# Kernel tuning notes

Measured on AMD Instinct MI355X. Metric: run time of the kernel, lower is better.

Reference implementation:

```python
import jax, jax.numpy as jnp
import numpy as np

N = 8192
MARGIN = 0.2
LAMB = 0.012
ITERS = 5


def setup_inputs() -> dict:
    key = jax.random.key(0)
    # sims in [0,1): cosine-similarity-like scores; exp(-(1-s)/lamb) needs s near [0,1]
    sims = jax.random.uniform(key, (N, N), dtype=jnp.float32)
    return {"sims": sims}


def _ot(sims):
    # Sinkhorn-Knopp normalization, r = c = ones so (r/u) == 1/u, (c/v) == 1/v
    P = jnp.exp(-(1.0 - sims) / LAMB)
    P = P / jnp.sum(P)  # global normalization (dims [-2,-1])
    for _ in range(ITERS):
        u = P.sum(axis=-1, keepdims=True)   # row sums  [N,1]
        P = P / u
        v = P.sum(axis=-2, keepdims=True)   # col sums  [1,N]
        P = P / v
    return P


def reference(sims):
    P = _ot(sims)
    d = jnp.diagonal(P)                     # [N]
    eye = jnp.eye(P.shape[0], dtype=bool)
    # cost_im: anchor = column diagonal (d[j]); cost_s: anchor = row diagonal (d[i])
    cost_im = jnp.where(eye, 0.0, jnp.maximum(P - d[None, :] + MARGIN, 0.0))
    cost_s = jnp.where(eye, 0.0, jnp.maximum(P - d[:, None] + MARGIN, 0.0))
    # max_violation = False -> sum over all hinge terms
    return cost_s.sum() + cost_im.sum()
```

## Files before the change

kernel.cpp:

```cpp
#include <hip/hip_runtime.h>


#define NN 8192u
#define MARGIN 0.2f
#define KF (1.4426950408889634f / 0.012f)

typedef float f32x4 __attribute__((ext_vector_type(4)));

__device__ __forceinline__ float wave_sum(float v) {
#pragma unroll
  for (int off = 32; off; off >>= 1) v += __shfl_down(v, off, 64);
  return v;
}


__global__ __launch_bounds__(256) void k_pass0(const float* __restrict__ sims,
                                               uint* __restrict__ Qd,
                                               float* __restrict__ R,
                                               float* __restrict__ qdiag,
                                               float* __restrict__ out) {
  __shared__ float red[4];
  const uint row = blockIdx.x, t = threadIdx.x;
  const uint lane = t & 63u, wid = t >> 6;
  if (row == 0u && t == 0u) *out = 0.f;
  float acc = 0.f;
#pragma unroll
  for (uint ch = 0; ch < 8u; ++ch) {
    const uint col0 = ch * 1024u + t * 4u;
    const f32x4 s = __builtin_nontemporal_load(
        (const f32x4*)(sims + (size_t)row * NN + col0));
    int p = 0;
    p = __builtin_amdgcn_cvt_pk_fp8_f32(exp2f((s[0] - 1.f) * KF),
                                        exp2f((s[1] - 1.f) * KF), p, false);
    p = __builtin_amdgcn_cvt_pk_fp8_f32(exp2f((s[2] - 1.f) * KF),
                                        exp2f((s[3] - 1.f) * KF), p, true);
    const uint up = (uint)p;
    Qd[((size_t)row * NN + col0) >> 2] = up;
    auto lo = __builtin_amdgcn_cvt_pk_f32_fp8(p, false);
    auto hi = __builtin_amdgcn_cvt_pk_f32_fp8(p, true);
    acc += (lo[0] + lo[1]) + (hi[0] + hi[1]);
    if (row - col0 < 4u)
      qdiag[row] = __builtin_amdgcn_cvt_f32_fp8(
          (int)((up >> ((row - col0) * 8u)) & 0xFFu), 0);
  }
  const float wacc = wave_sum(acc);
  if (lane == 0u) red[wid] = wacc;
  __syncthreads();
  if (t == 0u) R[row] = 1.f / (red[0] + red[1] + red[2] + red[3]);
}

__global__ __launch_bounds__(1024, 4) void k_fused(const uint* __restrict__ Qd,
                                                   float* __restrict__ Rg,
                                                   const float* __restrict__ Cg,
                                                   float* __restrict__ part,
                                                   int itx) {
  __shared__ float Rl[16];
  const uint b = blockIdx.x, t = threadIdx.x;
  const uint lane = t & 63u, w = t >> 6;
  const uint row0 = b * 16u;
  if (itx == 0) {
    if (t < 16u) Rl[t] = Rg[row0 + t];
  } else {
    const uint row = row0 + w;
    const uint* qr = Qd + (size_t)row * 2048u;
    float a = 0.f;
#pragma unroll 2
    for (uint m = 0; m < 8u; ++m) {
      const uint dw = m * 256u + lane * 4u;
      const uint4 q = *(const uint4*)(qr + dw);
      const float4* cp = (const float4*)(Cg + dw * 4u);
      const float4 c0 = cp[0], c1 = cp[1], c2 = cp[2], c3 = cp[3];
      auto l0 = __builtin_amdgcn_cvt_pk_f32_fp8((int)q.x, false);
      auto h0 = __builtin_amdgcn_cvt_pk_f32_fp8((int)q.x, true);
      a += l0[0] * c0.x + l0[1] * c0.y + h0[0] * c0.z + h0[1] * c0.w;
      auto l1 = __builtin_amdgcn_cvt_pk_f32_fp8((int)q.y, false);
      auto h1 = __builtin_amdgcn_cvt_pk_f32_fp8((int)q.y, true);
      a += l1[0] * c1.x + l1[1] * c1.y + h1[0] * c1.z + h1[1] * c1.w;
      auto l2 = __builtin_amdgcn_cvt_pk_f32_fp8((int)q.z, false);
      auto h2 = __builtin_amdgcn_cvt_pk_f32_fp8((int)q.z, true);
      a += l2[0] * c2.x + l2[1] * c2.y + h2[0] * c2.z + h2[1] * c2.w;
      auto l3 = __builtin_amdgcn_cvt_pk_f32_fp8((int)q.w, false);
      auto h3 = __builtin_amdgcn_cvt_pk_f32_fp8((int)q.w, true);
      a += l3[0] * c3.x + l3[1] * c3.y + h3[0] * c3.z + h3[1] * c3.w;
    }
    a = wave_sum(a);
    if (lane == 0u) {
      const float r = 1.f / a;
      Rg[row] = r;
      Rl[w] = r;
    }
  }
  __syncthreads();
  float a0 = 0.f, a1 = 0.f, a2 = 0.f, a3 = 0.f;
  float a4 = 0.f, a5 = 0.f, a6 = 0.f, a7 = 0.f;
  const uint cd = t * 2u;
#pragma unroll 4
  for (uint r = 0; r < 16u; ++r) {
    const float Rr = Rl[r];
    const uint2 q = *(const uint2*)(Qd + (size_t)(row0 + r) * 2048u + cd);
    auto lo = __builtin_amdgcn_cvt_pk_f32_fp8((int)q.x, false);
    auto hi = __builtin_amdgcn_cvt_pk_f32_fp8((int)q.x, true);
    a0 += lo[0] * Rr; a1 += lo[1] * Rr; a2 += hi[0] * Rr; a3 += hi[1] * Rr;
    lo = __builtin_amdgcn_cvt_pk_f32_fp8((int)q.y, false);
    hi = __builtin_amdgcn_cvt_pk_f32_fp8((int)q.y, true);
    a4 += lo[0] * Rr; a5 += lo[1] * Rr; a6 += hi[0] * Rr; a7 += hi[1] * Rr;
  }
  float* po = part + (size_t)b * NN + t * 8u;
  float4 o;
  o.x = a0; o.y = a1; o.z = a2; o.w = a3;
  *(float4*)(po) = o;
  o.x = a4; o.y = a5; o.z = a6; o.w = a7;
  *(float4*)(po + 4) = o;
}

__global__ __launch_bounds__(1024) void k_colred(const float* __restrict__ part,
                                                 float* __restrict__ C, int fin,
                                                 const float* __restrict__ R,
                                                 const float* __restrict__ qdiag,
                                                 float* __restrict__ dvec) {
  __shared__ float red2[3][256];
  const uint t = threadIdx.x;
  const uint lj = t & 255u;
  const uint q = t >> 8;
  const uint j = blockIdx.x * 256u + lj;
  float s = 0.f;
  const uint r0 = q * 128u;
#pragma unroll 8
  for (uint r = r0; r < r0 + 128u; ++r) s += part[(size_t)r * NN + j];
  if (q) red2[q - 1][lj] = s;
  __syncthreads();
  if (q == 0) {
    s += red2[0][lj] + red2[1][lj] + red2[2][lj];
    const float c = 1.f / s;
    C[j] = c;
    if (fin) dvec[j] = qdiag[j] * R[j] * c;
  }
}

__global__ __launch_bounds__(256) void k_loss(const uint* __restrict__ Qd,
                                              const float* __restrict__ R,
                                              const float* __restrict__ Cg,
                                              const float* __restrict__ dvec,
                                              float* __restrict__ out) {
  __shared__ float red[4];
  const uint t = threadIdx.x;
  const uint col = blockIdx.x * 1024u + t * 4u;
  const uint row0 = blockIdx.y * 128u;
  const float4 c4 = *(const float4*)(Cg + col);
  const float4 d4 = *(const float4*)(dvec + col);
  float acc = 0.f;
#pragma unroll 4
  for (uint rr = 0; rr < 128u; ++rr) {
    const uint row = row0 + rr;
    const float Rr = R[row];
    const float dr = dvec[row];
    const uint q = Qd[((size_t)row * NN + col) >> 2];
    auto lo = __builtin_amdgcn_cvt_pk_f32_fp8((int)q, false);
    auto hi = __builtin_amdgcn_cvt_pk_f32_fp8((int)q, true);
    float p, h;
    p = lo[0] * Rr * c4.x;
    h = fmaxf(p - d4.x + MARGIN, 0.f) + fmaxf(p - dr + MARGIN, 0.f);
    acc += (row == col + 0u) ? 0.f : h;
    p = lo[1] * Rr * c4.y;
    h = fmaxf(p - d4.y + MARGIN, 0.f) + fmaxf(p - dr + MARGIN, 0.f);
    acc += (row == col + 1u) ? 0.f : h;
    p = hi[0] * Rr * c4.z;
    h = fmaxf(p - d4.z + MARGIN, 0.f) + fmaxf(p - dr + MARGIN, 0.f);
    acc += (row == col + 2u) ? 0.f : h;
    p = hi[1] * Rr * c4.w;
    h = fmaxf(p - d4.w + MARGIN, 0.f) + fmaxf(p - dr + MARGIN, 0.f);
    acc += (row == col + 3u) ? 0.f : h;
  }
  const float v = wave_sum(acc);
  const uint lane = t & 63u, wid = t >> 6;
  if (lane == 0u) red[wid] = v;
  __syncthreads();
  if (t == 0u) atomicAdd(out, red[0] + red[1] + red[2] + red[3]);
}

static void run_fast(const float* sims, float* out, void* ws,
                     hipStream_t stream) {
  uint* Qd = (uint*)ws;
  float* part = (float*)(Qd + (size_t)NN * NN / 4u);
  float* R = part + 512u * (size_t)NN;
  float* C = R + NN;
  float* dv = C + NN;
  float* qd = dv + NN;

  k_pass0<<<8192, 256, 0, stream>>>(sims, Qd, R, qd, out);
  for (int it = 0; it < 5; ++it) {
    k_fused<<<512, 1024, 0, stream>>>(Qd, R, C, part, it);
    k_colred<<<32, 1024, 0, stream>>>(part, C, (it == 4) ? 1 : 0, R, qd, dv);
  }
  k_loss<<<dim3(8, 64), 256, 0, stream>>>(Qd, R, C, dv, out);
}


__global__ __launch_bounds__(256) void k_pass0d(const float* __restrict__ sims,
                                                float* __restrict__ R) {
  __shared__ float red[4];
  const uint row = blockIdx.x;
  const uint t = threadIdx.x;
  float acc = 0.f;
#pragma unroll
  for (uint ch = 0; ch < 8; ++ch) {
    const uint col = ch * 1024u + t * 4u;
    const float4 s = *(const float4*)(sims + (size_t)row * NN + col);
    acc += exp2f((s.x - 1.f) * KF) + exp2f((s.y - 1.f) * KF) +
           exp2f((s.z - 1.f) * KF) + exp2f((s.w - 1.f) * KF);
  }
  float v = wave_sum(acc);
  const int lane = threadIdx.x & 63, wid = threadIdx.x >> 6;
  if (lane == 0) red[wid] = v;
  __syncthreads();
  if (t == 0) R[row] = 1.f / (red[0] + red[1] + red[2] + red[3]);
}

__global__ __launch_bounds__(256) void k_colmvd(const float* __restrict__ sims,
                                                const float* __restrict__ R,
                                                float* __restrict__ part) {
  const uint t = threadIdx.x;
  const uint col = blockIdx.x * 1024u + t * 4u;
  const uint row0 = blockIdx.y * 64u;
  float a0 = 0.f, a1 = 0.f, a2 = 0.f, a3 = 0.f;
#pragma unroll 8
  for (uint rr = 0; rr < 64u; ++rr) {
    const uint row = row0 + rr;
    const float Rr = R[row];
    const float4 s = *(const float4*)(sims + (size_t)row * NN + col);
    a0 += exp2f((s.x - 1.f) * KF) * Rr;
    a1 += exp2f((s.y - 1.f) * KF) * Rr;
    a2 += exp2f((s.z - 1.f) * KF) * Rr;
    a3 += exp2f((s.w - 1.f) * KF) * Rr;
  }
  float4 o; o.x = a0; o.y = a1; o.z = a2; o.w = a3;
  *(float4*)(part + (size_t)blockIdx.y * NN + col) = o;
}

__global__ __launch_bounds__(1024) void k_colredd(
    const float* __restrict__ part, float* __restrict__ Cg, int fin,
    const float* __restrict__ sims, const float* __restrict__ R,
    float* __restrict__ dvec, float* __restrict__ out) {
  __shared__ float red2[3][256];
  const uint t = threadIdx.x;
  const uint lj = t & 255u;
  const uint q = t >> 8;
  const uint j = blockIdx.x * 256u + lj;
  float s = 0.f;
  const uint r0 = q * 32u;
#pragma unroll 8
  for (uint r = r0; r < r0 + 32u; ++r) s += part[(size_t)r * NN + j];
  if (q) red2[q - 1][lj] = s;
  __syncthreads();
  if (q == 0) {
    s += red2[0][lj] + red2[1][lj] + red2[2][lj];
    const float c = 1.f / s;
    Cg[j] = c;
    if (fin) {
      dvec[j] = exp2f((sims[(size_t)j * 8193u] - 1.f) * KF) * R[j] * c;
      if (j == 0) *out = 0.f;
    }
  }
}

__global__ __launch_bounds__(256) void k_rowmvd(const float* __restrict__ sims,
                                                const float* __restrict__ Cg,
                                                float* __restrict__ R) {
  __shared__ float red[4][4];
  const uint t = threadIdx.x;
  const uint row0 = blockIdx.x * 4u;
  float a0 = 0.f, a1 = 0.f, a2 = 0.f, a3 = 0.f;
#pragma unroll
  for (uint it = 0; it < 8u; ++it) {
    const uint col = it * 1024u + t * 4u;
    const float4 c = *(const float4*)(Cg + col);
    const float* sp = sims + (size_t)row0 * NN + col;
    const float4 s0 = *(const float4*)(sp);
    const float4 s1 = *(const float4*)(sp + NN);
    const float4 s2 = *(const float4*)(sp + 2u * NN);
    const float4 s3 = *(const float4*)(sp + 3u * NN);
    a0 += exp2f((s0.x - 1.f) * KF) * c.x + exp2f((s0.y - 1.f) * KF) * c.y +
          exp2f((s0.z - 1.f) * KF) * c.z + exp2f((s0.w - 1.f) * KF) * c.w;
    a1 += exp2f((s1.x - 1.f) * KF) * c.x + exp2f((s1.y - 1.f) * KF) * c.y +
          exp2f((s1.z - 1.f) * KF) * c.z + exp2f((s1.w - 1.f) * KF) * c.w;
    a2 += exp2f((s2.x - 1.f) * KF) * c.x + exp2f((s2.y - 1.f) * KF) * c.y +
          exp2f((s2.z - 1.f) * KF) * c.z + exp2f((s2.w - 1.f) * KF) * c.w;
    a3 += exp2f((s3.x - 1.f) * KF) * c.x + exp2f((s3.y - 1.f) * KF) * c.y +
          exp2f((s3.z - 1.f) * KF) * c.z + exp2f((s3.w - 1.f) * KF) * c.w;
  }
#pragma unroll
  for (int off = 32; off; off >>= 1) {
    a0 += __shfl_down(a0, off, 64);
    a1 += __shfl_down(a1, off, 64);
    a2 += __shfl_down(a2, off, 64);
    a3 += __shfl_down(a3, off, 64);
  }
  const uint lane = t & 63u, wid = t >> 6;
  if (lane == 0) {
    red[wid][0] = a0; red[wid][1] = a1; red[wid][2] = a2; red[wid][3] = a3;
  }
  __syncthreads();
  if (t < 4u)
    R[row0 + t] = 1.f / (red[0][t] + red[1][t] + red[2][t] + red[3][t]);
}

__global__ __launch_bounds__(256) void k_lossd(const float* __restrict__ sims,
                                               const float* __restrict__ R,
                                               const float* __restrict__ Cg,
                                               const float* __restrict__ dvec,
                                               float* __restrict__ out) {
  __shared__ float red[4];
  const uint t = threadIdx.x;
  const uint col = blockIdx.x * 1024u + t * 4u;
  const uint row0 = blockIdx.y * 128u;
  const float4 c4 = *(const float4*)(Cg + col);
  const float4 d4 = *(const float4*)(dvec + col);
  float acc = 0.f;
#pragma unroll 4
  for (uint rr = 0; rr < 128u; ++rr) {
    const uint row = row0 + rr;
    const float Rr = R[row];
    const float dr = dvec[row];
    const float4 s = *(const float4*)(sims + (size_t)row * NN + col);
    const float f0 = exp2f((s.x - 1.f) * KF);
    const float f1 = exp2f((s.y - 1.f) * KF);
    const float f2 = exp2f((s.z - 1.f) * KF);
    const float f3 = exp2f((s.w - 1.f) * KF);
    float p, h;
    p = f0 * Rr * c4.x;
    h = fmaxf(p - d4.x + MARGIN, 0.f) + fmaxf(p - dr + MARGIN, 0.f);
    acc += (row == col + 0u) ? 0.f : h;
    p = f1 * Rr * c4.y;
    h = fmaxf(p - d4.y + MARGIN, 0.f) + fmaxf(p - dr + MARGIN, 0.f);
    acc += (row == col + 1u) ? 0.f : h;
    p = f2 * Rr * c4.z;
    h = fmaxf(p - d4.z + MARGIN, 0.f) + fmaxf(p - dr + MARGIN, 0.f);
    acc += (row == col + 2u) ? 0.f : h;
    p = f3 * Rr * c4.w;
    h = fmaxf(p - d4.w + MARGIN, 0.f) + fmaxf(p - dr + MARGIN, 0.f);
    acc += (row == col + 3u) ? 0.f : h;
  }
  float v = wave_sum(acc);
  const int lane = threadIdx.x & 63, wid = threadIdx.x >> 6;
  if (lane == 0) red[wid] = v;
  __syncthreads();
  if (t == 0) atomicAdd(out, red[0] + red[1] + red[2] + red[3]);
}

static void run_dense(const float* sims, float* out, void* ws,
                      hipStream_t stream) {
  float* R = (float*)ws;
  float* C = R + NN;
  float* dv = C + NN;
  float* part = dv + NN;
  k_pass0d<<<8192, 256, 0, stream>>>(sims, R);
  for (int it = 0; it < 5; ++it) {
    k_colmvd<<<dim3(8, 128), 256, 0, stream>>>(sims, R, part);
    k_colredd<<<32, 1024, 0, stream>>>(part, C, (it == 4) ? 1 : 0, sims, R, dv,
                                       out);
    if (it < 4) k_rowmvd<<<2048, 256, 0, stream>>>(sims, C, R);
  }
  k_lossd<<<dim3(8, 64), 256, 0, stream>>>(sims, R, C, dv, out);
}


extern "C" void kernel_launch(void* const* d_in, const int* in_sizes, int n_in,
                              void* d_out, int out_size, void* d_ws,
                              size_t ws_size, hipStream_t stream) {
  const float* sims = (const float*)d_in[0];
  float* out = (float*)d_out;
  const size_t need_fast = (size_t)NN * NN +
                           (512u + 4u) * (size_t)NN * sizeof(float);
  if (ws_size >= need_fast) {
    run_fast(sims, out, d_ws, stream);
  } else {
    run_dense(sims, out, d_ws, stream);
  }
}
```

Before: 531.0 us.

## Replace fused row/column kernel and partial buffer with atomic column sums

Splits each Sinkhorn iteration into two kernels. A column matvec accumulates column sums directly into a double-buffered Csum array with atomicAdd and zeroes the other buffer for the next iteration. A separate row kernel computes reciprocal row sums. This removes the 512xN partial-sum buffer write and the column-reduction kernel, and folds the column reciprocals and the diagonal computation into the consumers. In exchange, the fp8 matrix is streamed twice per iteration instead of once with block-local reuse, and about a million float atomics are issued per iteration.

```diff
diff --git a/kernel.cpp b/kernel.cpp
--- a/kernel.cpp
+++ b/kernel.cpp
@@ -18,11 +18,13 @@
                                                uint* __restrict__ Qd,
                                                float* __restrict__ R,
                                                float* __restrict__ qdiag,
+                                               float* __restrict__ Csum0,
                                                float* __restrict__ out) {
   __shared__ float red[4];
   const uint row = blockIdx.x, t = threadIdx.x;
   const uint lane = t & 63u, wid = t >> 6;
   if (row == 0u && t == 0u) *out = 0.f;
+  if (row < 32u) Csum0[row * 256u + t] = 0.f;
   float acc = 0.f;
 #pragma unroll
   for (uint ch = 0; ch < 8u; ++ch) {
@@ -49,111 +51,102 @@
   if (t == 0u) R[row] = 1.f / (red[0] + red[1] + red[2] + red[3]);
 }
 
-__global__ __launch_bounds__(1024, 4) void k_fused(const uint* __restrict__ Qd,
-                                                   float* __restrict__ Rg,
-                                                   const float* __restrict__ Cg,
-                                                   float* __restrict__ part,
-                                                   int itx) {
-  __shared__ float Rl[16];
-  const uint b = blockIdx.x, t = threadIdx.x;
-  const uint lane = t & 63u, w = t >> 6;
-  const uint row0 = b * 16u;
-  if (itx == 0) {
-    if (t < 16u) Rl[t] = Rg[row0 + t];
-  } else {
-    const uint row = row0 + w;
-    const uint* qr = Qd + (size_t)row * 2048u;
-    float a = 0.f;
-#pragma unroll 2
-    for (uint m = 0; m < 8u; ++m) {
-      const uint dw = m * 256u + lane * 4u;
-      const uint4 q = *(const uint4*)(qr + dw);
-      const float4* cp = (const float4*)(Cg + dw * 4u);
-      const float4 c0 = cp[0], c1 = cp[1], c2 = cp[2], c3 = cp[3];
-      auto l0 = __builtin_amdgcn_cvt_pk_f32_fp8((int)q.x, false);
-      auto h0 = __builtin_amdgcn_cvt_pk_f32_fp8((int)q.x, true);
-      a += l0[0] * c0.x + l0[1] * c0.y + h0[0] * c0.z + h0[1] * c0.w;
-      auto l1 = __builtin_amdgcn_cvt_pk_f32_fp8((int)q.y, false);
-      auto h1 = __builtin_amdgcn_cvt_pk_f32_fp8((int)q.y, true);
-      a += l1[0] * c1.x + l1[1] * c1.y + h1[0] * c1.z + h1[1] * c1.w;
-      auto l2 = __builtin_amdgcn_cvt_pk_f32_fp8((int)q.z, false);
-      auto h2 = __builtin_amdgcn_cvt_pk_f32_fp8((int)q.z, true);
-      a += l2[0] * c2.x + l2[1] * c2.y + h2[0] * c2.z + h2[1] * c2.w;
-      auto l3 = __builtin_amdgcn_cvt_pk_f32_fp8((int)q.w, false);
-      auto h3 = __builtin_amdgcn_cvt_pk_f32_fp8((int)q.w, true);
-      a += l3[0] * c3.x + l3[1] * c3.y + h3[0] * c3.z + h3[1] * c3.w;
-    }
-    a = wave_sum(a);
-    if (lane == 0u) {
-      const float r = 1.f / a;
-      Rg[row] = r;
-      Rl[w] = r;
-    }
-  }
-  __syncthreads();
+__global__ __launch_bounds__(256) void k_colmv(const uint* __restrict__ Qd,
+                                               const float* __restrict__ R,
+                                               float* __restrict__ Csum,
+                                               float* __restrict__ CsumNext) {
+  const uint t = threadIdx.x;
+  const uint col = blockIdx.x * 1024u + t * 4u;
+  const uint row0 = blockIdx.y * 64u;
+  if (t < 8u) CsumNext[(blockIdx.y * 8u + blockIdx.x) * 8u + t] = 0.f;
   float a0 = 0.f, a1 = 0.f, a2 = 0.f, a3 = 0.f;
-  float a4 = 0.f, a5 = 0.f, a6 = 0.f, a7 = 0.f;
-  const uint cd = t * 2u;
-#pragma unroll 4
-  for (uint r = 0; r < 16u; ++r) {
-    const float Rr = Rl[r];
-    const uint2 q = *(const uint2*)(Qd + (size_t)(row0 + r) * 2048u + cd);
-    auto lo = __builtin_amdgcn_cvt_pk_f32_fp8((int)q.x, false);
-    auto hi = __builtin_amdgcn_cvt_pk_f32_fp8((int)q.x, true);
+#pragma unroll 8
+  for (uint rr = 0; rr < 64u; ++rr) {
+    const uint row = row0 + rr;
+    const float Rr = R[row];
+    const uint q = Qd[((size_t)row * NN + col) >> 2];
+    auto lo = __builtin_amdgcn_cvt_pk_f32_fp8((int)q, false);
+    auto hi = __builtin_amdgcn_cvt_pk_f32_fp8((int)q, true);
     a0 += lo[0] * Rr; a1 += lo[1] * Rr; a2 += hi[0] * Rr; a3 += hi[1] * Rr;
-    lo = __builtin_amdgcn_cvt_pk_f32_fp8((int)q.y, false);
-    hi = __builtin_amdgcn_cvt_pk_f32_fp8((int)q.y, true);
-    a4 += lo[0] * Rr; a5 += lo[1] * Rr; a6 += hi[0] * Rr; a7 += hi[1] * Rr;
-  }
-  float* po = part + (size_t)b * NN + t * 8u;
-  float4 o;
-  o.x = a0; o.y = a1; o.z = a2; o.w = a3;
-  *(float4*)(po) = o;
-  o.x = a4; o.y = a5; o.z = a6; o.w = a7;
-  *(float4*)(po + 4) = o;
-}
-
-__global__ __launch_bounds__(1024) void k_colred(const float* __restrict__ part,
-                                                 float* __restrict__ C, int fin,
-                                                 const float* __restrict__ R,
-                                                 const float* __restrict__ qdiag,
-                                                 float* __restrict__ dvec) {
-  __shared__ float red2[3][256];
-  const uint t = threadIdx.x;
-  const uint lj = t & 255u;
-  const uint q = t >> 8;
-  const uint j = blockIdx.x * 256u + lj;
-  float s = 0.f;
-  const uint r0 = q * 128u;
-#pragma unroll 8
-  for (uint r = r0; r < r0 + 128u; ++r) s += part[(size_t)r * NN + j];
-  if (q) red2[q - 1][lj] = s;
-  __syncthreads();
-  if (q == 0) {
-    s += red2[0][lj] + red2[1][lj] + red2[2][lj];
-    const float c = 1.f / s;
-    C[j] = c;
-    if (fin) dvec[j] = qdiag[j] * R[j] * c;
-  }
+  }
+  atomicAdd(&Csum[col + 0u], a0);
+  atomicAdd(&Csum[col + 1u], a1);
+  atomicAdd(&Csum[col + 2u], a2);
+  atomicAdd(&Csum[col + 3u], a3);
+}
+
+__global__ __launch_bounds__(256) void k_rowstep(const uint* __restrict__ Qd,
+                                                 const float* __restrict__ Csum,
+                                                 float* __restrict__ R) {
+  __shared__ float red[4][4];
+  const uint t = threadIdx.x;
+  const uint row0 = blockIdx.x * 4u;
+  float a0 = 0.f, a1 = 0.f, a2 = 0.f, a3 = 0.f;
+#pragma unroll
+  for (uint it = 0; it < 8u; ++it) {
+    const uint col = it * 1024u + t * 4u;
+    const float4 s = *(const float4*)(Csum + col);
+    float4 c;
+    c.x = 1.f / s.x; c.y = 1.f / s.y; c.z = 1.f / s.z; c.w = 1.f / s.w;
+    const uint base = (row0 * 2048u) + (col >> 2);
+    uint q = Qd[base];
+    auto lo = __builtin_amdgcn_cvt_pk_f32_fp8((int)q, false);
+    auto hi = __builtin_amdgcn_cvt_pk_f32_fp8((int)q, true);
+    a0 += lo[0] * c.x + lo[1] * c.y + hi[0] * c.z + hi[1] * c.w;
+    q = Qd[base + 2048u];
+    lo = __builtin_amdgcn_cvt_pk_f32_fp8((int)q, false);
+    hi = __builtin_amdgcn_cvt_pk_f32_fp8((int)q, true);
+    a1 += lo[0] * c.x + lo[1] * c.y + hi[0] * c.z + hi[1] * c.w;
+    q = Qd[base + 4096u];
+    lo = __builtin_amdgcn_cvt_pk_f32_fp8((int)q, false);
+    hi = __builtin_amdgcn_cvt_pk_f32_fp8((int)q, true);
+    a2 += lo[0] * c.x + lo[1] * c.y + hi[0] * c.z + hi[1] * c.w;
+    q = Qd[base + 6144u];
+    lo = __builtin_amdgcn_cvt_pk_f32_fp8((int)q, false);
+    hi = __builtin_amdgcn_cvt_pk_f32_fp8((int)q, true);
+    a3 += lo[0] * c.x + lo[1] * c.y + hi[0] * c.z + hi[1] * c.w;
+  }
+#pragma unroll
+  for (int off = 32; off; off >>= 1) {
+    a0 += __shfl_down(a0, off, 64);
+    a1 += __shfl_down(a1, off, 64);
+    a2 += __shfl_down(a2, off, 64);
+    a3 += __shfl_down(a3, off, 64);
+  }
+  const uint lane = t & 63u, wid = t >> 6;
+  if (lane == 0u) {
+    red[wid][0] = a0; red[wid][1] = a1; red[wid][2] = a2; red[wid][3] = a3;
+  }
+  __syncthreads();
+  if (t < 4u)
+    R[row0 + t] = 1.f / (red[0][t] + red[1][t] + red[2][t] + red[3][t]);
 }
 
 __global__ __launch_bounds__(256) void k_loss(const uint* __restrict__ Qd,
                                               const float* __restrict__ R,
-                                              const float* __restrict__ Cg,
-                                              const float* __restrict__ dvec,
+                                              const float* __restrict__ Csum,
+                                              const float* __restrict__ qdiag,
                                               float* __restrict__ out) {
   __shared__ float red[4];
   const uint t = threadIdx.x;
   const uint col = blockIdx.x * 1024u + t * 4u;
   const uint row0 = blockIdx.y * 128u;
-  const float4 c4 = *(const float4*)(Cg + col);
-  const float4 d4 = *(const float4*)(dvec + col);
+  const float4 cs = *(const float4*)(Csum + col);
+  float4 c4;
+  c4.x = 1.f / cs.x; c4.y = 1.f / cs.y; c4.z = 1.f / cs.z; c4.w = 1.f / cs.w;
+  const float4 r4 = *(const float4*)(R + col);
+  const float4 qd4 = *(const float4*)(qdiag + col);
+  float4 d4;
+  d4.x = qd4.x * r4.x * c4.x;
+  d4.y = qd4.y * r4.y * c4.y;
+  d4.z = qd4.z * r4.z * c4.z;
+  d4.w = qd4.w * r4.w * c4.w;
   float acc = 0.f;
 #pragma unroll 4
   for (uint rr = 0; rr < 128u; ++rr) {
     const uint row = row0 + rr;
     const float Rr = R[row];
-    const float dr = dvec[row];
+    const float dr = qdiag[row] * Rr * (1.f / Csum[row]);
     const uint q = Qd[((size_t)row * NN + col) >> 2];
     auto lo = __builtin_amdgcn_cvt_pk_f32_fp8((int)q, false);
     auto hi = __builtin_amdgcn_cvt_pk_f32_fp8((int)q, true);
@@ -181,18 +174,19 @@
 static void run_fast(const float* sims, float* out, void* ws,
                      hipStream_t stream) {
   uint* Qd = (uint*)ws;
-  float* part = (float*)(Qd + (size_t)NN * NN / 4u);
-  float* R = part + 512u * (size_t)NN;
-  float* C = R + NN;
-  float* dv = C + NN;
-  float* qd = dv + NN;
-
-  k_pass0<<<8192, 256, 0, stream>>>(sims, Qd, R, qd, out);
+  float* R = (float*)(Qd + (size_t)NN * NN / 4u);
+  float* qd = R + NN;
+  float* Csum0 = qd + NN;
+  float* Csum1 = Csum0 + NN;
+
+  k_pass0<<<8192, 256, 0, stream>>>(sims, Qd, R, qd, Csum0, out);
   for (int it = 0; it < 5; ++it) {
-    k_fused<<<512, 1024, 0, stream>>>(Qd, R, C, part, it);
-    k_colred<<<32, 1024, 0, stream>>>(part, C, (it == 4) ? 1 : 0, R, qd, dv);
-  }
-  k_loss<<<dim3(8, 64), 256, 0, stream>>>(Qd, R, C, dv, out);
+    float* A = (it & 1) ? Csum1 : Csum0;
+    float* B = (it & 1) ? Csum0 : Csum1;
+    k_colmv<<<dim3(8, 128), 256, 0, stream>>>(Qd, R, A, B);
+    if (it < 4) k_rowstep<<<2048, 256, 0, stream>>>(Qd, A, R);
+  }
+  k_loss<<<dim3(8, 64), 256, 0, stream>>>(Qd, R, Csum0, qd, out);
 }
 
 
@@ -369,8 +363,7 @@
                               size_t ws_size, hipStream_t stream) {
   const float* sims = (const float*)d_in[0];
   float* out = (float*)d_out;
-  const size_t need_fast = (size_t)NN * NN +
-                           (512u + 4u) * (size_t)NN * sizeof(float);
+  const size_t need_fast = (size_t)NN * NN + 4u * (size_t)NN * sizeof(float);
   if (ws_size >= need_fast) {
     run_fast(sims, out, d_ws, stream);
   } else {
```

Result: slower. 570.9 us (+7.5%).
